# Optimization experiments

Hardware: AMD Instinct MI355X
Metric: run time of the kernel (lower is better)

## Reference

```python
import jax, jax.numpy as jnp
import numpy as np

B, T, D = 4, 2048, 2048
H = 8            # num_heads (= num_kv_heads)
DK = D // H      # head_k_dim = 256
DV = D // H      # head_v_dim = 256
M = 64           # num_slots
GLN = 8.0        # gate_logit_normalizer
EPS = 1e-5
SCALE = 1.0


def swish(x):
    return x * jax.nn.sigmoid(x)


def rms_norm(x, w, eps=EPS):
    var = jnp.mean(jnp.square(x), axis=-1, keepdims=True)
    return x * jax.lax.rsqrt(var + eps) * w


def gsa_scan(q, k, v, s, g, scale):
    # q,k: [B,T,H,DK]; v: [B,T,H,DV]; s,g: [B,T,H,M]
    b, t, h, dk = q.shape
    dv = v.shape[-1]
    m = s.shape[-1]
    xs = tuple(jnp.moveaxis(a, 1, 0) for a in (q, k, v, s, g))  # time-major
    Hk0 = jnp.zeros((b, h, dk, m), q.dtype)
    Hv0 = jnp.zeros((b, h, m, dv), q.dtype)

    def step(carry, inp):
        Hk, Hv = carry
        qt, kt, vt, st, gt = inp
        dec = jnp.exp(gt)                                   # [B,H,M]
        # pass 1: K -> slot state, gate on slot (value) dim
        Hk = Hk * dec[:, :, None, :] + kt[..., :, None] * st[..., None, :]
        o1 = scale * jnp.einsum('bhd,bhdm->bhm', qt, Hk)
        qv = jax.nn.softmax(o1, axis=-1)                    # slot attention
        # pass 2: slot -> V state, gate on slot (key) dim
        Hv = Hv * dec[..., :, None] + st[..., :, None] * vt[..., None, :]
        ot = jnp.einsum('bhm,bhmv->bhv', qv, Hv)
        return (Hk, Hv), ot

    _, oT = jax.lax.scan(step, (Hk0, Hv0), xs)
    return jnp.moveaxis(oT, 0, 1)                           # [B,T,H,DV]


def setup_inputs() -> dict:
    key = jax.random.key(0)
    ks = jax.random.split(key, 8)
    gain = 2.0 ** (-2.5)

    def xavier(k, out_dim, in_dim):
        lim = gain * np.sqrt(6.0 / (in_dim + out_dim))
        return jax.random.uniform(k, (out_dim, in_dim), jnp.float32, -lim, lim)

    return {
        'hidden_states': jax.random.normal(ks[0], (B, T, D), jnp.float32),
        'norm_w': jnp.ones((D,), jnp.float32),
        'q_w': xavier(ks[1], D, D),
        'k_w': xavier(ks[2], D, D),
        'v_w': xavier(ks[3], D, D),
        'f_w': xavier(ks[4], H * M, D),
        'g_norm_w': jnp.ones((D,), jnp.float32),
        'o_w': xavier(ks[5], D, D),
    }


def reference(hidden_states, norm_w, q_w, k_w, v_w, f_w, g_norm_w, o_w):
    x = rms_norm(hidden_states, norm_w)
    q = jnp.einsum('btd,kd->btk', x, q_w).reshape(B, T, H, DK)
    k = jnp.einsum('btd,kd->btk', x, k_w).reshape(B, T, H, DK)
    v = jnp.einsum('btd,kd->btk', x, v_w).reshape(B, T, H, DV)
    f = jnp.einsum('btd,kd->btk', x, f_w).reshape(B, T, H, M)
    q, k = swish(q), swish(k)                 # swish feature map
    v = swish(v)
    f = jax.nn.log_sigmoid(f) / GLN           # log forget gates
    s = 1.0 - jnp.exp(f)                      # slot write strengths
    o = gsa_scan(q, k, v, s, f, SCALE)        # [B,T,H,DV]
    o = o.reshape(B, T, H * DV)
    o = rms_norm(swish(o), g_norm_w)
    return jnp.einsum('btd,kd->btk', o, o_w)
```

## Files before the change

kernel.cpp:

```cpp
#include <hip/hip_runtime.h>
#include <hip/hip_bf16.h>
#include <math.h>


typedef __bf16 bf16x8 __attribute__((ext_vector_type(8)));
typedef float f32x4 __attribute__((ext_vector_type(4)));

#define ROWS 8192
#define DM 2048

#define MODE_F32 0
#define MODE_SWISH 1
#define MODE_GATE 2

#define XS(r, c) ((c) ^ ((r) & 56))

__device__ __forceinline__ float u2f(unsigned short u) {
  union { unsigned int i; float f; } cv; cv.i = ((unsigned int)u) << 16; return cv.f;
}
__device__ __forceinline__ unsigned short f2us(float f) {
  return __builtin_bit_cast(unsigned short, __float2bfloat16(f));
}
__device__ __forceinline__ float swishf(float v) { return v / (1.f + expf(-v)); }

__device__ __forceinline__ void gload16(const void* g, void* l) {
  __builtin_amdgcn_global_load_lds(
      (const __attribute__((address_space(1))) void*)g,
      (__attribute__((address_space(3))) void*)l, 16, 0, 0);
}

__global__ __launch_bounds__(256) void xnorm_kernel(
    const float* __restrict__ in, const float* __restrict__ w,
    unsigned short* __restrict__ out)
{
  const int row = blockIdx.x, tid = threadIdx.x;
  const size_t base = (size_t)row * DM + tid * 8;
  float a[8];
#pragma unroll
  for (int i = 0; i < 8; ++i) a[i] = in[base + i];
  float ss = 0.f;
#pragma unroll
  for (int i = 0; i < 8; ++i) ss += a[i] * a[i];
#pragma unroll
  for (int off = 32; off; off >>= 1) ss += __shfl_xor(ss, off, 64);
  __shared__ float wsum[4];
  if ((tid & 63) == 0) wsum[tid >> 6] = ss;
  __syncthreads();
  float tot = wsum[0] + wsum[1] + wsum[2] + wsum[3];
  float rstd = rsqrtf(tot * (1.f / (float)DM) + 1e-5f);
#pragma unroll
  for (int i = 0; i < 8; ++i)
    out[base + i] = f2us(a[i] * rstd * w[tid * 8 + i]);
}

__global__ __launch_bounds__(256) void oact_norm_kernel(
    const float* __restrict__ o, const float* __restrict__ w,
    unsigned short* __restrict__ out)
{
  const int row = blockIdx.x, tid = threadIdx.x;
  const size_t base = (size_t)row * DM + tid * 8;
  float a[8];
#pragma unroll
  for (int i = 0; i < 8; ++i) a[i] = swishf(o[base + i]);
  float ss = 0.f;
#pragma unroll
  for (int i = 0; i < 8; ++i) ss += a[i] * a[i];
#pragma unroll
  for (int off = 32; off; off >>= 1) ss += __shfl_xor(ss, off, 64);
  __shared__ float wsum[4];
  if ((tid & 63) == 0) wsum[tid >> 6] = ss;
  __syncthreads();
  float tot = wsum[0] + wsum[1] + wsum[2] + wsum[3];
  float rstd = rsqrtf(tot * (1.f / (float)DM) + 1e-5f);
#pragma unroll
  for (int i = 0; i < 8; ++i)
    out[base + i] = f2us(a[i] * rstd * w[tid * 8 + i]);
}

__global__ __launch_bounds__(256) void wconv_kernel(
    const float* __restrict__ in, unsigned short* __restrict__ out)
{
  size_t i = ((size_t)blockIdx.x * 256 + threadIdx.x) * 8;
  float4 a = *(const float4*)(in + i);
  float4 b = *(const float4*)(in + i + 4);
  unsigned short u[8] = {f2us(a.x), f2us(a.y), f2us(a.z), f2us(a.w),
                         f2us(b.x), f2us(b.y), f2us(b.z), f2us(b.w)};
  *(uint4*)(out + i) = *(const uint4*)u;
}

__global__ __launch_bounds__(256) void mgemm2_kernel(
    const unsigned short* __restrict__ A, const unsigned short* __restrict__ WB,
    unsigned short* __restrict__ outB, float* __restrict__ outF,
    int N, int mode)
{
  __shared__ __align__(16) unsigned short As[128 * 32];
  __shared__ __align__(16) unsigned short Bs[128 * 32];
  const int bn = blockIdx.x, bm = blockIdx.y, tid = threadIdx.x;
  const int w = tid >> 6, l = tid & 63;
  const int wm = w & 1, wn = w >> 1;
  const int fr = l & 15, fq = l >> 4;

  f32x4 acc[4][4];
#pragma unroll
  for (int i = 0; i < 4; ++i)
#pragma unroll
    for (int j = 0; j < 4; ++j) acc[i][j] = (f32x4){0.f, 0.f, 0.f, 0.f};

  int prow[2], pcol[2];
#pragma unroll
  for (int j = 0; j < 2; ++j) {
    int p = w * 128 + j * 64 + l;
    prow[j] = p >> 2;
    pcol[j] = ((p & 3) ^ ((prow[j] >> 1) & 3)) * 8;
  }
  const size_t abase = (size_t)(bm * 128) * DM;
  const size_t bbase = (size_t)(bn * 128) * DM;

  for (int k0 = 0; k0 < DM; k0 += 32) {
#pragma unroll
    for (int j = 0; j < 2; ++j) {
      gload16(A + abase + (size_t)prow[j] * DM + k0 + pcol[j],
              &As[(w * 128 + j * 64) * 8]);
      gload16(WB + bbase + (size_t)prow[j] * DM + k0 + pcol[j],
              &Bs[(w * 128 + j * 64) * 8]);
    }
    __syncthreads();
    bf16x8 af[4], bfr[4];
#pragma unroll
    for (int i = 0; i < 4; ++i) {
      int row = wm * 64 + i * 16 + fr;
      af[i] = *(const bf16x8*)&As[row * 32 + ((fq ^ ((row >> 1) & 3)) * 8)];
    }
#pragma unroll
    for (int j = 0; j < 4; ++j) {
      int row = wn * 64 + j * 16 + fr;
      bfr[j] = *(const bf16x8*)&Bs[row * 32 + ((fq ^ ((row >> 1) & 3)) * 8)];
    }
#pragma unroll
    for (int i = 0; i < 4; ++i)
#pragma unroll
      for (int j = 0; j < 4; ++j)
        acc[i][j] = __builtin_amdgcn_mfma_f32_16x16x32_bf16(af[i], bfr[j], acc[i][j], 0, 0, 0);
    __syncthreads();
  }

#pragma unroll
  for (int i = 0; i < 4; ++i) {
#pragma unroll
    for (int rr = 0; rr < 4; ++rr) {
      int row = bm * 128 + wm * 64 + i * 16 + fq * 4 + rr;
#pragma unroll
      for (int j = 0; j < 4; ++j) {
        int col = bn * 128 + wn * 64 + j * 16 + fr;
        float val = acc[i][j][rr];
        size_t idx = (size_t)row * N + col;
        if (mode == MODE_SWISH)      outB[idx] = f2us(swishf(val));
        else if (mode == MODE_F32)   outF[idx] = val;
        else {
          float ls = fminf(val, 0.f) - log1pf(expf(-fabsf(val)));
          outF[idx] = ls * 0.125f;
        }
      }
    }
  }
}

#define BM 128
#define BN 128
#define BK 32
#define LDSP 40

__global__ __launch_bounds__(256) void mgemm_kernel(
    const unsigned short* __restrict__ A, const float* __restrict__ W,
    unsigned short* __restrict__ outB, float* __restrict__ outF,
    int N, int mode)
{
  __shared__ __align__(16) unsigned short As[BM][LDSP];
  __shared__ __align__(16) unsigned short Bs[BN][LDSP];
  const int bn = blockIdx.x, bm = blockIdx.y, tid = threadIdx.x;
  const int w = tid >> 6, l = tid & 63;
  const int wm = w & 1, wn = w >> 1;
  const int fr = l & 15, fq = l >> 4;

  f32x4 acc[4][4];
#pragma unroll
  for (int i = 0; i < 4; ++i)
#pragma unroll
    for (int j = 0; j < 4; ++j) acc[i][j] = (f32x4){0.f, 0.f, 0.f, 0.f};

  for (int k0 = 0; k0 < DM; k0 += BK) {
#pragma unroll
    for (int s = 0; s < 2; ++s) {
      int chunk = tid + s * 256;
      int row = chunk >> 2;
      int cc = (chunk & 3) * 8;
      *(uint4*)&As[row][cc] =
          *(const uint4*)(A + (size_t)(bm * BM + row) * DM + k0 + cc);
    }
#pragma unroll
    for (int s = 0; s < 4; ++s) {
      int chunk = tid + s * 256;
      int row = chunk >> 3;
      int cc = (chunk & 7) * 4;
      float4 wv = *(const float4*)(W + (size_t)(bn * BN + row) * DM + k0 + cc);
      ushort4 w4;
      w4.x = f2us(wv.x); w4.y = f2us(wv.y); w4.z = f2us(wv.z); w4.w = f2us(wv.w);
      *(ushort4*)&Bs[row][cc] = w4;
    }
    __syncthreads();
    bf16x8 af[4], bfr[4];
#pragma unroll
    for (int i = 0; i < 4; ++i) af[i] = *(const bf16x8*)&As[wm * 64 + i * 16 + fr][fq * 8];
#pragma unroll
    for (int j = 0; j < 4; ++j) bfr[j] = *(const bf16x8*)&Bs[wn * 64 + j * 16 + fr][fq * 8];
#pragma unroll
    for (int i = 0; i < 4; ++i)
#pragma unroll
      for (int j = 0; j < 4; ++j)
        acc[i][j] = __builtin_amdgcn_mfma_f32_16x16x32_bf16(af[i], bfr[j], acc[i][j], 0, 0, 0);
    __syncthreads();
  }

#pragma unroll
  for (int i = 0; i < 4; ++i) {
#pragma unroll
    for (int rr = 0; rr < 4; ++rr) {
      int row = bm * BM + wm * 64 + i * 16 + fq * 4 + rr;
#pragma unroll
      for (int j = 0; j < 4; ++j) {
        int col = bn * BN + wn * 64 + j * 16 + fr;
        float val = acc[i][j][rr];
        size_t idx = (size_t)row * N + col;
        if (mode == MODE_SWISH)      outB[idx] = f2us(swishf(val));
        else if (mode == MODE_F32)   outF[idx] = val;
        else {
          float ls = fminf(val, 0.f) - log1pf(expf(-fabsf(val)));
          outF[idx] = ls * 0.125f;
        }
      }
    }
  }
}

template<int NCH, bool INIT>
__global__ __launch_bounds__(512) void gsa_chunk_t(
    const unsigned short* __restrict__ Q, const unsigned short* __restrict__ K,
    const unsigned short* __restrict__ V, const float* __restrict__ G,
    float* __restrict__ O, const float* __restrict__ DK,
    const float* __restrict__ DV)
{
  __shared__ __align__(16) char pool[158848];
  auto EB   = (unsigned short(*)[72])(pool + 0);
  auto O1B  = (unsigned short(*)[72])(pool + 9216);
  auto RB   = (unsigned short(*)[72])(pool + 18432);
  auto RT   = (unsigned short(*)[72])(pool + 27648);
  auto SB   = (unsigned short(*)[72])(pool + 36864);
  auto UB   = (unsigned short(*)[72])(pool + 46080);
  float (*GS)[64] = (float(*)[64])(pool + 55296);
  auto QT   = (unsigned short(*)[264])(pool + 55296);
  auto KTt2 = (unsigned short(*)[72])(pool + 55296);
  auto VTt2 = (unsigned short(*)[72])(pool + 55296);
  auto KT   = (unsigned short(*)[264])(pool + 89088);
  auto VTt1 = (unsigned short(*)[72])(pool + 89088);
  auto GkB  = (unsigned short(*)[264])(pool + 122880);
  auto KTt1 = (unsigned short(*)[72])(pool + 122880);
  auto GvB1 = (unsigned short(*)[72])(pool + 122880);
  auto GvB2 = (unsigned short(*)[72])(pool + 9216);
  float (*red)[68] = (float(*)[68])(pool + 156672);

  int bh, seg;
  if constexpr (INIT) { bh = (int)blockIdx.x >> 3; seg = (int)blockIdx.x & 7; }
  else                { bh = (int)blockIdx.x; seg = 0; }
  const int b = bh >> 3, h = bh & 7;
  const int tid = threadIdx.x;
  const int w = tid >> 6, l = tid & 63, fr = l & 15, fq = l >> 4;
  const int wlo = w & 3, whi = w >> 2;

  f32x4 gk[8], gv[8];
  if constexpr (INIT) {
    const float* dk = DK + ((size_t)bh * 8 + seg) * 16384;
    const float* dv = DV + ((size_t)bh * 8 + seg) * 16384;
#pragma unroll
    for (int jj = 0; jj < 8; ++jj) {
      int ut = (w >= 4 ? 8 : 0) + wlo * 2 + (jj >> 2);
#pragma unroll
      for (int rr = 0; rr < 4; ++rr) {
        gk[jj][rr] = dk[(wlo * 16 + fq * 4 + rr) * 256 + (whi * 8 + jj) * 16 + fr];
        gv[jj][rr] = dv[(ut * 16 + fq * 4 + rr) * 64 + (jj & 3) * 16 + fr];
      }
    }
  } else {
#pragma unroll
    for (int jj = 0; jj < 8; ++jj) {
      gk[jj] = (f32x4){0.f, 0.f, 0.f, 0.f};
      gv[jj] = (f32x4){0.f, 0.f, 0.f, 0.f};
    }
  }

  for (int cl = 0; cl < NCH; ++cl) {
    const int c = seg * NCH + cl;
    const int rowbase = b * 2048 + c * 64;
    const bool upd = (cl != NCH - 1);

#pragma unroll
    for (int s = 0; s < 2; ++s) {
      int id = s * 512 + tid, row = id >> 4, mq = id & 15;
      *(float4*)&GS[row][mq * 4] =
          *(const float4*)&G[(size_t)(rowbase + row) * 512 + h * 64 + mq * 4];
    }
#pragma unroll
    for (int jj = 0; jj < 8; ++jj) {
      int dcol = (whi * 8 + jj) * 16 + fr;
#pragma unroll
      for (int rr = 0; rr < 4; ++rr) {
        int grow = wlo * 16 + fq * 4 + rr;
        GkB[grow][XS(grow, dcol)] = f2us(gk[jj][rr]);
      }
    }
    __syncthreads();

    {
      float ps = 0.f;
#pragma unroll
      for (int j = 0; j < 8; ++j) ps += GS[w * 8 + j][l];
      red[w][l] = ps;
    }
    __syncthreads();

    {
      float cum = 0.f;
      for (int g2 = 0; g2 < w; ++g2) cum += red[g2][l];
#pragma unroll
      for (int j = 0; j < 8; ++j) {
        int i = w * 8 + j;
        float gval = GS[i][l];
        cum += gval;
        float e = expf(cum);
        float s_ = 1.f - expf(gval);
        float r_ = s_ / e;
        EB[i][l] = f2us(e);
        RB[i][XS(i, l)] = f2us(r_);
        RT[l][XS(l, i)] = f2us(r_);
      }
    }
    __syncthreads();

#pragma unroll
    for (int s = 0; s < 4; ++s) {
      int id = s * 512 + tid, row = id >> 5, cc = (id & 31) * 8;
      int sc = XS(row, cc);
      size_t gb = (size_t)(rowbase + row) * 2048 + h * 256 + cc;
      *(uint4*)&QT[row][sc] = *(const uint4*)(Q + gb);
      *(uint4*)&KT[row][sc] = *(const uint4*)(K + gb);
    }
    __syncthreads();

    f32x4 o1acc[2];
    o1acc[0] = (f32x4){0.f, 0.f, 0.f, 0.f};
    o1acc[1] = (f32x4){0.f, 0.f, 0.f, 0.f};
    {
      f32x4 sacc[2];
      sacc[0] = (f32x4){0.f, 0.f, 0.f, 0.f};
      sacc[1] = (f32x4){0.f, 0.f, 0.f, 0.f};
      int ar_ = wlo * 16 + fr;
#pragma unroll
      for (int kk = 0; kk < 8; ++kk) {
        bf16x8 aq = *(const bf16x8*)&QT[ar_][XS(ar_, kk * 32 + fq * 8)];
#pragma unroll
        for (int t2 = 0; t2 < 2; ++t2) {
          int tj = (whi + 2 * t2) * 16 + fr;
          int bc = XS(tj, kk * 32 + fq * 8);
          bf16x8 bk = *(const bf16x8*)&KT[tj][bc];
          sacc[t2] = __builtin_amdgcn_mfma_f32_16x16x32_bf16(aq, bk, sacc[t2], 0, 0, 0);
          bf16x8 bg = *(const bf16x8*)&GkB[tj][bc];
          o1acc[t2] = __builtin_amdgcn_mfma_f32_16x16x32_bf16(aq, bg, o1acc[t2], 0, 0, 0);
        }
      }
#pragma unroll
      for (int t2 = 0; t2 < 2; ++t2)
#pragma unroll
        for (int rr = 0; rr < 4; ++rr) {
          int i = wlo * 16 + fq * 4 + rr;
          int tau = (whi + 2 * t2) * 16 + fr;
          SB[i][XS(i, tau)] = f2us(tau <= i ? sacc[t2][rr] : 0.f);
        }
    }
    __syncthreads();

    {
      int ar_ = wlo * 16 + fr;
#pragma unroll
      for (int kk = 0; kk < 2; ++kk) {
        bf16x8 as = *(const bf16x8*)&SB[ar_][XS(ar_, kk * 32 + fq * 8)];
#pragma unroll
        for (int t2 = 0; t2 < 2; ++t2) {
          int tj = (whi + 2 * t2) * 16 + fr;
          bf16x8 br = *(const bf16x8*)&RT[tj][XS(tj, kk * 32 + fq * 8)];
          o1acc[t2] = __builtin_amdgcn_mfma_f32_16x16x32_bf16(as, br, o1acc[t2], 0, 0, 0);
        }
      }
#pragma unroll
      for (int t2 = 0; t2 < 2; ++t2)
#pragma unroll
        for (int rr = 0; rr < 4; ++rr) {
          int i = wlo * 16 + fq * 4 + rr;
          int m = (whi + 2 * t2) * 16 + fr;
          O1B[i][XS(i, m)] = f2us(u2f(EB[i][m]) * o1acc[t2][rr]);
        }
    }
    __syncthreads();

    {
      int i = tid >> 3, mq = tid & 7;
      int sc = XS(i, mq * 8);
      uint4 raw = *(const uint4*)&O1B[i][sc];
      const unsigned short* rp = (const unsigned short*)&raw;
      float x[8];
#pragma unroll
      for (int j = 0; j < 8; ++j) x[j] = u2f(rp[j]);
      float mx = x[0];
#pragma unroll
      for (int j = 1; j < 8; ++j) mx = fmaxf(mx, x[j]);
      mx = fmaxf(mx, __shfl_xor(mx, 1, 64));
      mx = fmaxf(mx, __shfl_xor(mx, 2, 64));
      mx = fmaxf(mx, __shfl_xor(mx, 4, 64));
      float ex[8], sum = 0.f;
#pragma unroll
      for (int j = 0; j < 8; ++j) { ex[j] = expf(x[j] - mx); sum += ex[j]; }
      sum += __shfl_xor(sum, 1, 64);
      sum += __shfl_xor(sum, 2, 64);
      sum += __shfl_xor(sum, 4, 64);
      float inv = 1.f / sum;
      unsigned short up[8];
#pragma unroll
      for (int j = 0; j < 8; ++j)
        up[j] = f2us(ex[j] * inv * u2f(EB[i][mq * 8 + j]));
      *(uint4*)&UB[i][sc] = *(uint4*)up;
    }
    {
      int m2 = tid >> 3, tq = tid & 7;
      int sc = XS(m2, tq * 8);
      float e63 = u2f(EB[63][m2]);
      uint4 raw = *(const uint4*)&RT[m2][sc];
      const unsigned short* rp = (const unsigned short*)&raw;
      unsigned short ow[8];
#pragma unroll
      for (int j = 0; j < 8; ++j) ow[j] = f2us(u2f(rp[j]) * e63);
      *(uint4*)&RT[m2][sc] = *(uint4*)ow;
    }
    __syncthreads();

    {
      f32x4 pacc[2];
      pacc[0] = (f32x4){0.f, 0.f, 0.f, 0.f};
      pacc[1] = (f32x4){0.f, 0.f, 0.f, 0.f};
      int ar_ = wlo * 16 + fr;
#pragma unroll
      for (int kk = 0; kk < 2; ++kk) {
        bf16x8 ar = *(const bf16x8*)&RB[ar_][XS(ar_, kk * 32 + fq * 8)];
#pragma unroll
        for (int t2 = 0; t2 < 2; ++t2) {
          int tj = (whi + 2 * t2) * 16 + fr;
          bf16x8 bu = *(const bf16x8*)&UB[tj][XS(tj, kk * 32 + fq * 8)];
          pacc[t2] = __builtin_amdgcn_mfma_f32_16x16x32_bf16(ar, bu, pacc[t2], 0, 0, 0);
        }
      }
#pragma unroll
      for (int t2 = 0; t2 < 2; ++t2)
#pragma unroll
        for (int rr = 0; rr < 4; ++rr) {
          int tau = wlo * 16 + fq * 4 + rr;
          int i = (whi + 2 * t2) * 16 + fr;
          SB[i][XS(i, tau)] = f2us(tau <= i ? pacc[t2][rr] : 0.f);
        }
    }
    if (upd) {
#pragma unroll
      for (int s = 0; s < 2; ++s) {
        int id = s * 512 + tid, d8 = id & 15, tau = id >> 4;
        uint4 raw = *(const uint4*)&KT[tau][XS(tau, d8 * 8)];
        const unsigned short* rp = (const unsigned short*)&raw;
#pragma unroll
        for (int j = 0; j < 8; ++j) {
          int trow = d8 * 8 + j;
          KTt1[trow][XS(trow, tau)] = rp[j];
        }
      }
    }
    __syncthreads();

    if (upd) {
      if (w < 4) {
        float e63r[4];
#pragma unroll
        for (int rr = 0; rr < 4; ++rr) e63r[rr] = u2f(EB[63][wlo * 16 + fq * 4 + rr]);
        int wr = wlo * 16 + fr;
        bf16x8 aw0 = *(const bf16x8*)&RT[wr][XS(wr, fq * 8)];
        bf16x8 aw1 = *(const bf16x8*)&RT[wr][XS(wr, 32 + fq * 8)];
#pragma unroll
        for (int jj = 0; jj < 8; ++jj) {
#pragma unroll
          for (int rr = 0; rr < 4; ++rr) gk[jj][rr] *= e63r[rr];
          int kr = jj * 16 + fr;
          bf16x8 bk0 = *(const bf16x8*)&KTt1[kr][XS(kr, fq * 8)];
          bf16x8 bk1 = *(const bf16x8*)&KTt1[kr][XS(kr, 32 + fq * 8)];
          gk[jj] = __builtin_amdgcn_mfma_f32_16x16x32_bf16(aw0, bk0, gk[jj], 0, 0, 0);
          gk[jj] = __builtin_amdgcn_mfma_f32_16x16x32_bf16(aw1, bk1, gk[jj], 0, 0, 0);
        }
      } else {
#pragma unroll
        for (int s = 0; s < 4; ++s) {
          int id = s * 256 + (tid - 256), d8 = id & 15, tau = id >> 4;
          uint4 raw = *(const uint4*)&KT[tau][XS(tau, 128 + d8 * 8)];
          const unsigned short* rp = (const unsigned short*)&raw;
#pragma unroll
          for (int j = 0; j < 8; ++j) {
            int trow = d8 * 8 + j;
            KTt2[trow][XS(trow, tau)] = rp[j];
          }
        }
      }
    }
    __syncthreads();

    if (upd && w >= 4) {
      float e63r[4];
#pragma unroll
      for (int rr = 0; rr < 4; ++rr) e63r[rr] = u2f(EB[63][wlo * 16 + fq * 4 + rr]);
      int wr = wlo * 16 + fr;
      bf16x8 aw0 = *(const bf16x8*)&RT[wr][XS(wr, fq * 8)];
      bf16x8 aw1 = *(const bf16x8*)&RT[wr][XS(wr, 32 + fq * 8)];
#pragma unroll
      for (int jj = 0; jj < 8; ++jj) {
#pragma unroll
        for (int rr = 0; rr < 4; ++rr) gk[jj][rr] *= e63r[rr];
        int kr = jj * 16 + fr;
        bf16x8 bk0 = *(const bf16x8*)&KTt2[kr][XS(kr, fq * 8)];
        bf16x8 bk1 = *(const bf16x8*)&KTt2[kr][XS(kr, 32 + fq * 8)];
        gk[jj] = __builtin_amdgcn_mfma_f32_16x16x32_bf16(aw0, bk0, gk[jj], 0, 0, 0);
        gk[jj] = __builtin_amdgcn_mfma_f32_16x16x32_bf16(aw1, bk1, gk[jj], 0, 0, 0);
      }
    }
    if (w < 4) {
#pragma unroll
      for (int s = 0; s < 4; ++s) {
        int id = s * 256 + tid, u8 = id & 15, tau = id >> 4;
        uint4 raw = *(const uint4*)(V + (size_t)(rowbase + tau) * 2048 + h * 256 + u8 * 8);
        const unsigned short* rp = (const unsigned short*)&raw;
#pragma unroll
        for (int j = 0; j < 8; ++j) {
          int trow = u8 * 8 + j;
          VTt1[trow][XS(trow, tau)] = rp[j];
        }
      }
#pragma unroll
      for (int jj = 0; jj < 8; ++jj) {
        int u0 = (wlo * 2 + (jj >> 2)) * 16 + fq * 4;
        int m = (jj & 3) * 16 + fr;
#pragma unroll
        for (int rr = 0; rr < 4; ++rr) {
          int grow = u0 + rr;
          GvB1[grow][XS(grow, m)] = f2us(gv[jj][rr]);
        }
      }
    }
    __syncthreads();

    {
      int pr = wlo * 16 + fr;
      bf16x8 ap0 = *(const bf16x8*)&SB[pr][XS(pr, fq * 8)];
      bf16x8 ap1 = *(const bf16x8*)&SB[pr][XS(pr, 32 + fq * 8)];
      bf16x8 au0 = *(const bf16x8*)&UB[pr][XS(pr, fq * 8)];
      bf16x8 au1 = *(const bf16x8*)&UB[pr][XS(pr, 32 + fq * 8)];
#pragma unroll
      for (int oo = 0; oo < 4; ++oo) {
        int ut = whi * 4 + oo;
        int vr = ut * 16 + fr;
        f32x4 oa = (f32x4){0.f, 0.f, 0.f, 0.f};
        bf16x8 bv0 = *(const bf16x8*)&VTt1[vr][XS(vr, fq * 8)];
        bf16x8 bv1 = *(const bf16x8*)&VTt1[vr][XS(vr, 32 + fq * 8)];
        bf16x8 bg0 = *(const bf16x8*)&GvB1[vr][XS(vr, fq * 8)];
        bf16x8 bg1 = *(const bf16x8*)&GvB1[vr][XS(vr, 32 + fq * 8)];
        oa = __builtin_amdgcn_mfma_f32_16x16x32_bf16(ap0, bv0, oa, 0, 0, 0);
        oa = __builtin_amdgcn_mfma_f32_16x16x32_bf16(ap1, bv1, oa, 0, 0, 0);
        oa = __builtin_amdgcn_mfma_f32_16x16x32_bf16(au0, bg0, oa, 0, 0, 0);
        oa = __builtin_amdgcn_mfma_f32_16x16x32_bf16(au1, bg1, oa, 0, 0, 0);
#pragma unroll
        for (int rr = 0; rr < 4; ++rr)
          O[(size_t)(rowbase + wlo * 16 + fq * 4 + rr) * 2048 + h * 256 + ut * 16 + fr] = oa[rr];
      }
    }
#pragma unroll
    for (int s = 0; s < 2; ++s) {
      int id = s * 512 + tid, u8 = id & 15, tau = id >> 4;
      uint4 raw = *(const uint4*)(V + (size_t)(rowbase + tau) * 2048 + h * 256 + 128 + u8 * 8);
      const unsigned short* rp = (const unsigned short*)&raw;
#pragma unroll
      for (int j = 0; j < 8; ++j) {
        int trow = u8 * 8 + j;
        VTt2[trow][XS(trow, tau)] = rp[j];
      }
    }
    if (w < 4) {
      if (upd) {
#pragma unroll
        for (int jj = 0; jj < 8; ++jj) {
          int ut = wlo * 2 + (jj >> 2), mt = jj & 3;
          float e63v = u2f(EB[63][mt * 16 + fr]);
#pragma unroll
          for (int rr = 0; rr < 4; ++rr) gv[jj][rr] *= e63v;
          int vr = ut * 16 + fr, br_ = mt * 16 + fr;
          bf16x8 av0 = *(const bf16x8*)&VTt1[vr][XS(vr, fq * 8)];
          bf16x8 av1 = *(const bf16x8*)&VTt1[vr][XS(vr, 32 + fq * 8)];
          bf16x8 bw0 = *(const bf16x8*)&RT[br_][XS(br_, fq * 8)];
          bf16x8 bw1 = *(const bf16x8*)&RT[br_][XS(br_, 32 + fq * 8)];
          gv[jj] = __builtin_amdgcn_mfma_f32_16x16x32_bf16(av0, bw0, gv[jj], 0, 0, 0);
          gv[jj] = __builtin_amdgcn_mfma_f32_16x16x32_bf16(av1, bw1, gv[jj], 0, 0, 0);
        }
      }
    } else {
#pragma unroll
      for (int jj = 0; jj < 8; ++jj) {
        int u0 = (wlo * 2 + (jj >> 2)) * 16 + fq * 4;
        int m = (jj & 3) * 16 + fr;
#pragma unroll
        for (int rr = 0; rr < 4; ++rr) {
          int grow = u0 + rr;
          GvB2[grow][XS(grow, m)] = f2us(gv[jj][rr]);
        }
      }
    }
    __syncthreads();

    {
      int pr = wlo * 16 + fr;
      bf16x8 ap0 = *(const bf16x8*)&SB[pr][XS(pr, fq * 8)];
      bf16x8 ap1 = *(const bf16x8*)&SB[pr][XS(pr, 32 + fq * 8)];
      bf16x8 au0 = *(const bf16x8*)&UB[pr][XS(pr, fq * 8)];
      bf16x8 au1 = *(const bf16x8*)&UB[pr][XS(pr, 32 + fq * 8)];
#pragma unroll
      for (int oo = 0; oo < 4; ++oo) {
        int utl = whi * 4 + oo;
        int vr = utl * 16 + fr;
        f32x4 oa = (f32x4){0.f, 0.f, 0.f, 0.f};
        bf16x8 bv0 = *(const bf16x8*)&VTt2[vr][XS(vr, fq * 8)];
        bf16x8 bv1 = *(const bf16x8*)&VTt2[vr][XS(vr, 32 + fq * 8)];
        bf16x8 bg0 = *(const bf16x8*)&GvB2[vr][XS(vr, fq * 8)];
        bf16x8 bg1 = *(const bf16x8*)&GvB2[vr][XS(vr, 32 + fq * 8)];
        oa = __builtin_amdgcn_mfma_f32_16x16x32_bf16(ap0, bv0, oa, 0, 0, 0);
        oa = __builtin_amdgcn_mfma_f32_16x16x32_bf16(ap1, bv1, oa, 0, 0, 0);
        oa = __builtin_amdgcn_mfma_f32_16x16x32_bf16(au0, bg0, oa, 0, 0, 0);
        oa = __builtin_amdgcn_mfma_f32_16x16x32_bf16(au1, bg1, oa, 0, 0, 0);
#pragma unroll
        for (int rr = 0; rr < 4; ++rr)
          O[(size_t)(rowbase + wlo * 16 + fq * 4 + rr) * 2048 + h * 256 + 128 + utl * 16 + fr] = oa[rr];
      }
    }
    if (upd && w >= 4) {
#pragma unroll
      for (int jj = 0; jj < 8; ++jj) {
        int utl = wlo * 2 + (jj >> 2), mt = jj & 3;
        float e63v = u2f(EB[63][mt * 16 + fr]);
#pragma unroll
        for (int rr = 0; rr < 4; ++rr) gv[jj][rr] *= e63v;
        int vr = utl * 16 + fr, br_ = mt * 16 + fr;
        bf16x8 av0 = *(const bf16x8*)&VTt2[vr][XS(vr, fq * 8)];
        bf16x8 av1 = *(const bf16x8*)&VTt2[vr][XS(vr, 32 + fq * 8)];
        bf16x8 bw0 = *(const bf16x8*)&RT[br_][XS(br_, fq * 8)];
        bf16x8 bw1 = *(const bf16x8*)&RT[br_][XS(br_, 32 + fq * 8)];
        gv[jj] = __builtin_amdgcn_mfma_f32_16x16x32_bf16(av0, bw0, gv[jj], 0, 0, 0);
        gv[jj] = __builtin_amdgcn_mfma_f32_16x16x32_bf16(av1, bw1, gv[jj], 0, 0, 0);
      }
    }
    __syncthreads();
  }
}

__global__ __launch_bounds__(512) void gsa_segA_kernel(
    const unsigned short* __restrict__ K, const unsigned short* __restrict__ V,
    const float* __restrict__ G, float* __restrict__ DK, float* __restrict__ DV,
    float* __restrict__ ES)
{
  __shared__ __align__(16) char pool[135552];
  float (*GS)[64] = (float(*)[64])(pool);
  float (*red)[68] = (float(*)[68])(pool + 16384);
  auto RT   = (unsigned short(*)[72])(pool + 18560);
  float* e63f = (float*)(pool + 27776);
  auto KT   = (unsigned short(*)[264])(pool + 28032);
  auto KTt1 = (unsigned short(*)[72])(pool + 61824);
  auto KTt2 = (unsigned short(*)[72])(pool + 80256);
  auto VTt1 = (unsigned short(*)[72])(pool + 98688);
  auto VTt2 = (unsigned short(*)[72])(pool + 117120);

  const int bh = (int)blockIdx.x >> 3, seg = (int)blockIdx.x & 7;
  const int b = bh >> 3, h = bh & 7;
  const int tid = threadIdx.x;
  const int w = tid >> 6, l = tid & 63, fr = l & 15, fq = l >> 4;
  const int wlo = w & 3, whi = w >> 2;

  f32x4 gk[8], gv[8];
#pragma unroll
  for (int jj = 0; jj < 8; ++jj) {
    gk[jj] = (f32x4){0.f, 0.f, 0.f, 0.f};
    gv[jj] = (f32x4){0.f, 0.f, 0.f, 0.f};
  }
  float gsum = 0.f;

  for (int cl = 0; cl < 4; ++cl) {
    const int rowbase = b * 2048 + (seg * 4 + cl) * 64;

#pragma unroll
    for (int s = 0; s < 2; ++s) {
      int id = s * 512 + tid, row = id >> 4, mq = id & 15;
      *(float4*)&GS[row][mq * 4] =
          *(const float4*)&G[(size_t)(rowbase + row) * 512 + h * 64 + mq * 4];
    }
#pragma unroll
    for (int s = 0; s < 4; ++s) {
      int id = s * 512 + tid, row = id >> 5, cc = (id & 31) * 8;
      *(uint4*)&KT[row][XS(row, cc)] =
          *(const uint4*)(K + (size_t)(rowbase + row) * 2048 + h * 256 + cc);
    }
    __syncthreads();

    {
      float ps = 0.f;
#pragma unroll
      for (int j = 0; j < 8; ++j) ps += GS[w * 8 + j][l];
      red[w][l] = ps;
    }
    __syncthreads();

    {
      float cum = 0.f;
      for (int g2 = 0; g2 < w; ++g2) cum += red[g2][l];
#pragma unroll
      for (int j = 0; j < 8; ++j) {
        int i = w * 8 + j;
        float gval = GS[i][l];
        cum += gval;
        float e = expf(cum);
        float r_ = (1.f - expf(gval)) / e;
        RT[l][XS(l, i)] = f2us(r_);
      }
      if (w == 7) { gsum += cum; e63f[l] = expf(cum); }
    }
    __syncthreads();

    {
      int m2 = tid >> 3, tq = tid & 7;
      int sc = XS(m2, tq * 8);
      float e63 = e63f[m2];
      uint4 raw = *(const uint4*)&RT[m2][sc];
      const unsigned short* rp = (const unsigned short*)&raw;
      unsigned short ow[8];
#pragma unroll
      for (int j = 0; j < 8; ++j) ow[j] = f2us(u2f(rp[j]) * e63);
      *(uint4*)&RT[m2][sc] = *(uint4*)ow;
    }
#pragma unroll
    for (int s = 0; s < 2; ++s) {
      int id = s * 512 + tid, d8 = id & 15, tau = id >> 4;
      uint4 raw1 = *(const uint4*)&KT[tau][XS(tau, d8 * 8)];
      uint4 raw2 = *(const uint4*)&KT[tau][XS(tau, 128 + d8 * 8)];
      const unsigned short* rp1 = (const unsigned short*)&raw1;
      const unsigned short* rp2 = (const unsigned short*)&raw2;
#pragma unroll
      for (int j = 0; j < 8; ++j) {
        int trow = d8 * 8 + j;
        KTt1[trow][XS(trow, tau)] = rp1[j];
        KTt2[trow][XS(trow, tau)] = rp2[j];
      }
    }
#pragma unroll
    for (int s = 0; s < 2; ++s) {
      int id = s * 512 + tid, u8 = id & 15, tau = id >> 4;
      size_t gb = (size_t)(rowbase + tau) * 2048 + h * 256 + u8 * 8;
      uint4 raw1 = *(const uint4*)(V + gb);
      uint4 raw2 = *(const uint4*)(V + gb + 128);
      const unsigned short* rp1 = (const unsigned short*)&raw1;
      const unsigned short* rp2 = (const unsigned short*)&raw2;
#pragma unroll
      for (int j = 0; j < 8; ++j) {
        int trow = u8 * 8 + j;
        VTt1[trow][XS(trow, tau)] = rp1[j];
        VTt2[trow][XS(trow, tau)] = rp2[j];
      }
    }
    __syncthreads();

    {
      float e63r[4];
#pragma unroll
      for (int rr = 0; rr < 4; ++rr) e63r[rr] = e63f[wlo * 16 + fq * 4 + rr];
      int wr = wlo * 16 + fr;
      bf16x8 aw0 = *(const bf16x8*)&RT[wr][XS(wr, fq * 8)];
      bf16x8 aw1 = *(const bf16x8*)&RT[wr][XS(wr, 32 + fq * 8)];
      auto KTx = (w < 4) ? KTt1 : KTt2;
#pragma unroll
      for (int jj = 0; jj < 8; ++jj) {
#pragma unroll
        for (int rr = 0; rr < 4; ++rr) gk[jj][rr] *= e63r[rr];
        int kr = jj * 16 + fr;
        bf16x8 bk0 = *(const bf16x8*)&KTx[kr][XS(kr, fq * 8)];
        bf16x8 bk1 = *(const bf16x8*)&KTx[kr][XS(kr, 32 + fq * 8)];
        gk[jj] = __builtin_amdgcn_mfma_f32_16x16x32_bf16(aw0, bk0, gk[jj], 0, 0, 0);
        gk[jj] = __builtin_amdgcn_mfma_f32_16x16x32_bf16(aw1, bk1, gk[jj], 0, 0, 0);
      }
      auto VTx = (w < 4) ? VTt1 : VTt2;
#pragma unroll
      for (int jj = 0; jj < 8; ++jj) {
        int utl = wlo * 2 + (jj >> 2), mt = jj & 3;
        float e63v = e63f[mt * 16 + fr];
#pragma unroll
        for (int rr = 0; rr < 4; ++rr) gv[jj][rr] *= e63v;
        int vr = utl * 16 + fr, br_ = mt * 16 + fr;
        bf16x8 av0 = *(const bf16x8*)&VTx[vr][XS(vr, fq * 8)];
        bf16x8 av1 = *(const bf16x8*)&VTx[vr][XS(vr, 32 + fq * 8)];
        bf16x8 bw0 = *(const bf16x8*)&RT[br_][XS(br_, fq * 8)];
        bf16x8 bw1 = *(const bf16x8*)&RT[br_][XS(br_, 32 + fq * 8)];
        gv[jj] = __builtin_amdgcn_mfma_f32_16x16x32_bf16(av0, bw0, gv[jj], 0, 0, 0);
        gv[jj] = __builtin_amdgcn_mfma_f32_16x16x32_bf16(av1, bw1, gv[jj], 0, 0, 0);
      }
    }
    __syncthreads();
  }

  float* dk = DK + ((size_t)bh * 8 + seg) * 16384;
  float* dv = DV + ((size_t)bh * 8 + seg) * 16384;
#pragma unroll
  for (int jj = 0; jj < 8; ++jj) {
    int ut = (w >= 4 ? 8 : 0) + wlo * 2 + (jj >> 2);
#pragma unroll
    for (int rr = 0; rr < 4; ++rr) {
      dk[(wlo * 16 + fq * 4 + rr) * 256 + (whi * 8 + jj) * 16 + fr] = gk[jj][rr];
      dv[(ut * 16 + fq * 4 + rr) * 64 + (jj & 3) * 16 + fr] = gv[jj][rr];
    }
  }
  if (w == 7) ES[((size_t)bh * 8 + seg) * 64 + l] = expf(gsum);
}

__global__ __launch_bounds__(1024) void gsa_segB_kernel(
    float* __restrict__ DK, float* __restrict__ DV, const float* __restrict__ ES)
{
  const int bh = blockIdx.x, tid = threadIdx.x;
  __shared__ float es[8][64];
  if (tid < 512) es[tid >> 6][tid & 63] = ES[(size_t)bh * 512 + tid];
  __syncthreads();
  float* dk = DK + (size_t)bh * 8 * 16384;
  float* dv = DV + (size_t)bh * 8 * 16384;
  for (int k = 0; k < 16; ++k) {
    int e = k * 1024 + tid;
    int m = e >> 8;
    float S = 0.f;
#pragma unroll
    for (int s = 0; s < 8; ++s) {
      float d = dk[s * 16384 + e];
      dk[s * 16384 + e] = S;
      S = fmaf(S, es[s][m], d);
    }
  }
  for (int k = 0; k < 16; ++k) {
    int e = k * 1024 + tid;
    int m = e & 63;
    float S = 0.f;
#pragma unroll
    for (int s = 0; s < 8; ++s) {
      float d = dv[s * 16384 + e];
      dv[s * 16384 + e] = S;
      S = fmaf(S, es[s][m], d);
    }
  }
}

__global__ __launch_bounds__(256) void fillf_kernel(float* o, float v) {
  o[(size_t)blockIdx.x * 256 + threadIdx.x] = v;
}

extern "C" void kernel_launch(void* const* d_in, const int* in_sizes, int n_in,
                              void* d_out, int out_size, void* d_ws, size_t ws_size,
                              hipStream_t stream)
{
  const float* hidden   = (const float*)d_in[0];
  const float* norm_w   = (const float*)d_in[1];
  const float* q_w      = (const float*)d_in[2];
  const float* k_w      = (const float*)d_in[3];
  const float* v_w      = (const float*)d_in[4];
  const float* f_w      = (const float*)d_in[5];
  const float* g_norm_w = (const float*)d_in[6];
  const float* o_w      = (const float*)d_in[7];

  float* dout = (float*)d_out;
  char* ws = (char*)d_ws;
  const size_t SZB = (size_t)ROWS * DM * 2;
  const size_t SZG = (size_t)ROWS * 512 * 4;
  const size_t NEED = 4 * SZB + SZG;
  const size_t SZD = (size_t)32 * 8 * 16384 * 4;
  const size_t NEED_BIG = NEED + 2 * SZD + (size_t)32 * 8 * 64 * 4;
  const size_t SZWB = (size_t)DM * DM * 2;
  const size_t SZWF = (size_t)512 * DM * 2;
  const size_t NEED_W = NEED_BIG + 4 * SZWB + SZWF;

  if (ws_size < NEED) {
    fillf_kernel<<<65536, 256, 0, stream>>>(dout, 123.0f);
    return;
  }

  unsigned short* XN = (unsigned short*)(ws);
  unsigned short* Qb = (unsigned short*)(ws + SZB);
  unsigned short* Kb = (unsigned short*)(ws + 2 * SZB);
  unsigned short* Vb = (unsigned short*)(ws + 3 * SZB);
  float* Gb          = (float*)(ws + 4 * SZB);
  float* DK          = (float*)(ws + NEED);
  float* DV          = DK + (size_t)32 * 8 * 16384;
  float* ES          = DV + (size_t)32 * 8 * 16384;
  unsigned short* WQ = (unsigned short*)(ws + NEED_BIG);
  unsigned short* WK = WQ + SZWB / 2;
  unsigned short* WV = WK + SZWB / 2;
  unsigned short* WO = WV + SZWB / 2;
  unsigned short* WF = WO + SZWB / 2;

  xnorm_kernel<<<ROWS, 256, 0, stream>>>(hidden, norm_w, XN);

  if (ws_size >= NEED_W) {
    wconv_kernel<<<2048, 256, 0, stream>>>(q_w, WQ);
    wconv_kernel<<<2048, 256, 0, stream>>>(k_w, WK);
    wconv_kernel<<<2048, 256, 0, stream>>>(v_w, WV);
    wconv_kernel<<<2048, 256, 0, stream>>>(o_w, WO);
    wconv_kernel<<<512, 256, 0, stream>>>(f_w, WF);

    mgemm2_kernel<<<dim3(16, 64), 256, 0, stream>>>(XN, WQ, Qb, nullptr, 2048, MODE_SWISH);
    mgemm2_kernel<<<dim3(16, 64), 256, 0, stream>>>(XN, WK, Kb, nullptr, 2048, MODE_SWISH);
    mgemm2_kernel<<<dim3(16, 64), 256, 0, stream>>>(XN, WV, Vb, nullptr, 2048, MODE_SWISH);
    mgemm2_kernel<<<dim3(4, 64), 256, 0, stream>>>(XN, WF, nullptr, Gb, 512, MODE_GATE);
  } else {
    mgemm_kernel<<<dim3(16, 64), 256, 0, stream>>>(XN, q_w, Qb, nullptr, 2048, MODE_SWISH);
    mgemm_kernel<<<dim3(16, 64), 256, 0, stream>>>(XN, k_w, Kb, nullptr, 2048, MODE_SWISH);
    mgemm_kernel<<<dim3(16, 64), 256, 0, stream>>>(XN, v_w, Vb, nullptr, 2048, MODE_SWISH);
    mgemm_kernel<<<dim3(4, 64), 256, 0, stream>>>(XN, f_w, nullptr, Gb, 512, MODE_GATE);
  }

  if (ws_size >= NEED_BIG) {
    gsa_segA_kernel<<<256, 512, 0, stream>>>(Kb, Vb, Gb, DK, DV, ES);
    gsa_segB_kernel<<<32, 1024, 0, stream>>>(DK, DV, ES);
    gsa_chunk_t<4, true><<<256, 512, 0, stream>>>(Qb, Kb, Vb, Gb, dout, DK, DV);
  } else {
    gsa_chunk_t<32, false><<<32, 512, 0, stream>>>(Qb, Kb, Vb, Gb, dout, nullptr, nullptr);
  }

  oact_norm_kernel<<<ROWS, 256, 0, stream>>>(dout, g_norm_w, XN);

  if (ws_size >= NEED_W)
    mgemm2_kernel<<<dim3(16, 64), 256, 0, stream>>>(XN, WO, nullptr, dout, 2048, MODE_F32);
  else
    mgemm_kernel<<<dim3(16, 64), 256, 0, stream>>>(XN, o_w, nullptr, dout, 2048, MODE_F32);
}
```

Before: 946.6 us.

## Prefetch next chunk's Q/K/V/G into registers and swizzle GEMM block order

```diff
diff --git a/kernel.cpp b/kernel.cpp
--- a/kernel.cpp
+++ b/kernel.cpp
@@ -95,7 +95,12 @@
 {
   __shared__ __align__(16) unsigned short As[128 * 32];
   __shared__ __align__(16) unsigned short Bs[128 * 32];
-  const int bn = blockIdx.x, bm = blockIdx.y, tid = threadIdx.x;
+  const int tid = threadIdx.x;
+  const int bid = (int)(blockIdx.y * gridDim.x + blockIdx.x);
+  const int nwg = (int)(gridDim.x * gridDim.y);
+  const int cpx = nwg >> 3;
+  const int swz = (bid & 7) * cpx + (bid >> 3);
+  const int bn = swz % (int)gridDim.x, bm = swz / (int)gridDim.x;
   const int w = tid >> 6, l = tid & 63;
   const int wm = w & 1, wn = w >> 1;
   const int fr = l & 15, fq = l >> 4;
@@ -276,6 +281,46 @@
   const int w = tid >> 6, l = tid & 63, fr = l & 15, fq = l >> 4;
   const int wlo = w & 3, whi = w >> 2;
 
+  float4 pg[2];
+  uint4 pq[4], pk[4], pv1[4], pv2[2];
+  auto pref_g = [&](int c) {
+    const int rb = b * 2048 + c * 64;
+#pragma unroll
+    for (int s = 0; s < 2; ++s) {
+      int id = s * 512 + tid, row = id >> 4, mq = id & 15;
+      pg[s] = *(const float4*)&G[(size_t)(rb + row) * 512 + h * 64 + mq * 4];
+    }
+  };
+  auto pref_qk = [&](int c) {
+    const int rb = b * 2048 + c * 64;
+#pragma unroll
+    for (int s = 0; s < 4; ++s) {
+      int id = s * 512 + tid, row = id >> 5, cc = (id & 31) * 8;
+      size_t gb = (size_t)(rb + row) * 2048 + h * 256 + cc;
+      pq[s] = *(const uint4*)(Q + gb);
+      pk[s] = *(const uint4*)(K + gb);
+    }
+  };
+  auto pref_v = [&](int c) {
+    const int rb = b * 2048 + c * 64;
+    if (tid < 256) {
+#pragma unroll
+      for (int s = 0; s < 4; ++s) {
+        int id = s * 256 + tid, u8 = id & 15, tau = id >> 4;
+        pv1[s] = *(const uint4*)(V + (size_t)(rb + tau) * 2048 + h * 256 + u8 * 8);
+      }
+    }
+#pragma unroll
+    for (int s = 0; s < 2; ++s) {
+      int id = s * 512 + tid, u8 = id & 15, tau = id >> 4;
+      pv2[s] = *(const uint4*)(V + (size_t)(rb + tau) * 2048 + h * 256 + 128 + u8 * 8);
+    }
+  };
+
+  pref_g(seg * NCH);
+  pref_qk(seg * NCH);
+  pref_v(seg * NCH);
+
   f32x4 gk[8], gv[8];
   if constexpr (INIT) {
     const float* dk = DK + ((size_t)bh * 8 + seg) * 16384;
@@ -305,8 +350,7 @@
 #pragma unroll
     for (int s = 0; s < 2; ++s) {
       int id = s * 512 + tid, row = id >> 4, mq = id & 15;
-      *(float4*)&GS[row][mq * 4] =
-          *(const float4*)&G[(size_t)(rowbase + row) * 512 + h * 64 + mq * 4];
+      *(float4*)&GS[row][mq * 4] = pg[s];
     }
 #pragma unroll
     for (int jj = 0; jj < 8; ++jj) {
@@ -349,11 +393,12 @@
     for (int s = 0; s < 4; ++s) {
       int id = s * 512 + tid, row = id >> 5, cc = (id & 31) * 8;
       int sc = XS(row, cc);
-      size_t gb = (size_t)(rowbase + row) * 2048 + h * 256 + cc;
-      *(uint4*)&QT[row][sc] = *(const uint4*)(Q + gb);
-      *(uint4*)&KT[row][sc] = *(const uint4*)(K + gb);
-    }
-    __syncthreads();
+      *(uint4*)&QT[row][sc] = pq[s];
+      *(uint4*)&KT[row][sc] = pk[s];
+    }
+    __syncthreads();
+
+    if (cl + 1 < NCH) { pref_g(c + 1); pref_qk(c + 1); }
 
     f32x4 o1acc[2];
     o1acc[0] = (f32x4){0.f, 0.f, 0.f, 0.f};
@@ -545,8 +590,7 @@
 #pragma unroll
       for (int s = 0; s < 4; ++s) {
         int id = s * 256 + tid, u8 = id & 15, tau = id >> 4;
-        uint4 raw = *(const uint4*)(V + (size_t)(rowbase + tau) * 2048 + h * 256 + u8 * 8);
-        const unsigned short* rp = (const unsigned short*)&raw;
+        const unsigned short* rp = (const unsigned short*)&pv1[s];
 #pragma unroll
         for (int j = 0; j < 8; ++j) {
           int trow = u8 * 8 + j;
@@ -593,14 +637,14 @@
 #pragma unroll
     for (int s = 0; s < 2; ++s) {
       int id = s * 512 + tid, u8 = id & 15, tau = id >> 4;
-      uint4 raw = *(const uint4*)(V + (size_t)(rowbase + tau) * 2048 + h * 256 + 128 + u8 * 8);
-      const unsigned short* rp = (const unsigned short*)&raw;
+      const unsigned short* rp = (const unsigned short*)&pv2[s];
 #pragma unroll
       for (int j = 0; j < 8; ++j) {
         int trow = u8 * 8 + j;
         VTt2[trow][XS(trow, tau)] = rp[j];
       }
     }
+    if (cl + 1 < NCH) pref_v(c + 1);
     if (w < 4) {
       if (upd) {
 #pragma unroll
@@ -698,6 +742,34 @@
   const int w = tid >> 6, l = tid & 63, fr = l & 15, fq = l >> 4;
   const int wlo = w & 3, whi = w >> 2;
 
+  float4 pg[2];
+  uint4 pk[4], pv[4];
+  auto pref_gk = [&](int cl) {
+    const int rb = b * 2048 + (seg * 4 + cl) * 64;
+#pragma unroll
+    for (int s = 0; s < 2; ++s) {
+      int id = s * 512 + tid, row = id >> 4, mq = id & 15;
+      pg[s] = *(const float4*)&G[(size_t)(rb + row) * 512 + h * 64 + mq * 4];
+    }
+#pragma unroll
+    for (int s = 0; s < 4; ++s) {
+      int id = s * 512 + tid, row = id >> 5, cc = (id & 31) * 8;
+      pk[s] = *(const uint4*)(K + (size_t)(rb + row) * 2048 + h * 256 + cc);
+    }
+  };
+  auto pref_v = [&](int cl) {
+    const int rb = b * 2048 + (seg * 4 + cl) * 64;
+#pragma unroll
+    for (int s = 0; s < 2; ++s) {
+      int id = s * 512 + tid, u8 = id & 15, tau = id >> 4;
+      size_t gb = (size_t)(rb + tau) * 2048 + h * 256 + u8 * 8;
+      pv[s * 2]     = *(const uint4*)(V + gb);
+      pv[s * 2 + 1] = *(const uint4*)(V + gb + 128);
+    }
+  };
+  pref_gk(0);
+  pref_v(0);
+
   f32x4 gk[8], gv[8];
 #pragma unroll
   for (int jj = 0; jj < 8; ++jj) {
@@ -707,21 +779,19 @@
   float gsum = 0.f;
 
   for (int cl = 0; cl < 4; ++cl) {
-    const int rowbase = b * 2048 + (seg * 4 + cl) * 64;
-
 #pragma unroll
     for (int s = 0; s < 2; ++s) {
       int id = s * 512 + tid, row = id >> 4, mq = id & 15;
-      *(float4*)&GS[row][mq * 4] =
-          *(const float4*)&G[(size_t)(rowbase + row) * 512 + h * 64 + mq * 4];
+      *(float4*)&GS[row][mq * 4] = pg[s];
     }
 #pragma unroll
     for (int s = 0; s < 4; ++s) {
       int id = s * 512 + tid, row = id >> 5, cc = (id & 31) * 8;
-      *(uint4*)&KT[row][XS(row, cc)] =
-          *(const uint4*)(K + (size_t)(rowbase + row) * 2048 + h * 256 + cc);
-    }
-    __syncthreads();
+      *(uint4*)&KT[row][XS(row, cc)] = pk[s];
+    }
+    __syncthreads();
+
+    if (cl + 1 < 4) pref_gk(cl + 1);
 
     {
       float ps = 0.f;
@@ -775,11 +845,8 @@
 #pragma unroll
     for (int s = 0; s < 2; ++s) {
       int id = s * 512 + tid, u8 = id & 15, tau = id >> 4;
-      size_t gb = (size_t)(rowbase + tau) * 2048 + h * 256 + u8 * 8;
-      uint4 raw1 = *(const uint4*)(V + gb);
-      uint4 raw2 = *(const uint4*)(V + gb + 128);
-      const unsigned short* rp1 = (const unsigned short*)&raw1;
-      const unsigned short* rp2 = (const unsigned short*)&raw2;
+      const unsigned short* rp1 = (const unsigned short*)&pv[s * 2];
+      const unsigned short* rp2 = (const unsigned short*)&pv[s * 2 + 1];
 #pragma unroll
       for (int j = 0; j < 8; ++j) {
         int trow = u8 * 8 + j;
@@ -787,6 +854,7 @@
         VTt2[trow][XS(trow, tau)] = rp2[j];
       }
     }
+    if (cl + 1 < 4) pref_v(cl + 1);
     __syncthreads();
 
     {
```

Result: slower. 1.024 ms (+8.2%).

## Fuse Q/K/V/gate projection GEMMs into one launch with XCD-aware block swizzle

Applied to the files above, without the earlier changes.

```diff
diff --git a/kernel.cpp b/kernel.cpp
--- a/kernel.cpp
+++ b/kernel.cpp
@@ -95,7 +95,12 @@
 {
   __shared__ __align__(16) unsigned short As[128 * 32];
   __shared__ __align__(16) unsigned short Bs[128 * 32];
-  const int bn = blockIdx.x, bm = blockIdx.y, tid = threadIdx.x;
+  const int tid = threadIdx.x;
+  const int bid = (int)(blockIdx.y * gridDim.x + blockIdx.x);
+  const int nwg = (int)(gridDim.x * gridDim.y);
+  const int cpx = nwg >> 3;
+  const int swz = (bid & 7) * cpx + (bid >> 3);
+  const int bn = swz % (int)gridDim.x, bm = swz / (int)gridDim.x;
   const int w = tid >> 6, l = tid & 63;
   const int wm = w & 1, wn = w >> 1;
   const int fr = l & 15, fq = l >> 4;
@@ -159,6 +164,91 @@
         else {
           float ls = fminf(val, 0.f) - log1pf(expf(-fabsf(val)));
           outF[idx] = ls * 0.125f;
+        }
+      }
+    }
+  }
+}
+
+__global__ __launch_bounds__(256) void mgemm2_fused_kernel(
+    const unsigned short* __restrict__ A, const unsigned short* __restrict__ WALL,
+    unsigned short* __restrict__ Qb, unsigned short* __restrict__ Kb,
+    unsigned short* __restrict__ Vb, float* __restrict__ Gb)
+{
+  __shared__ __align__(16) unsigned short As[128 * 32];
+  __shared__ __align__(16) unsigned short Bs[128 * 32];
+  const int tid = threadIdx.x;
+  const int bid = (int)(blockIdx.y * gridDim.x + blockIdx.x);
+  const int nwg = (int)(gridDim.x * gridDim.y);
+  const int cpx = nwg >> 3;
+  const int swz = (bid & 7) * cpx + (bid >> 3);
+  const int bn = swz % (int)gridDim.x, bm = swz / (int)gridDim.x;
+  const int w = tid >> 6, l = tid & 63;
+  const int wm = w & 1, wn = w >> 1;
+  const int fr = l & 15, fq = l >> 4;
+
+  f32x4 acc[4][4];
+#pragma unroll
+  for (int i = 0; i < 4; ++i)
+#pragma unroll
+    for (int j = 0; j < 4; ++j) acc[i][j] = (f32x4){0.f, 0.f, 0.f, 0.f};
+
+  int prow[2], pcol[2];
+#pragma unroll
+  for (int j = 0; j < 2; ++j) {
+    int p = w * 128 + j * 64 + l;
+    prow[j] = p >> 2;
+    pcol[j] = ((p & 3) ^ ((prow[j] >> 1) & 3)) * 8;
+  }
+  const size_t abase = (size_t)(bm * 128) * DM;
+  const size_t bbase = (size_t)(bn * 128) * DM;
+
+  for (int k0 = 0; k0 < DM; k0 += 32) {
+#pragma unroll
+    for (int j = 0; j < 2; ++j) {
+      gload16(A + abase + (size_t)prow[j] * DM + k0 + pcol[j],
+              &As[(w * 128 + j * 64) * 8]);
+      gload16(WALL + bbase + (size_t)prow[j] * DM + k0 + pcol[j],
+              &Bs[(w * 128 + j * 64) * 8]);
+    }
+    __syncthreads();
+    bf16x8 af[4], bfr[4];
+#pragma unroll
+    for (int i = 0; i < 4; ++i) {
+      int row = wm * 64 + i * 16 + fr;
+      af[i] = *(const bf16x8*)&As[row * 32 + ((fq ^ ((row >> 1) & 3)) * 8)];
+    }
+#pragma unroll
+    for (int j = 0; j < 4; ++j) {
+      int row = wn * 64 + j * 16 + fr;
+      bfr[j] = *(const bf16x8*)&Bs[row * 32 + ((fq ^ ((row >> 1) & 3)) * 8)];
+    }
+#pragma unroll
+    for (int i = 0; i < 4; ++i)
+#pragma unroll
+      for (int j = 0; j < 4; ++j)
+        acc[i][j] = __builtin_amdgcn_mfma_f32_16x16x32_bf16(af[i], bfr[j], acc[i][j], 0, 0, 0);
+    __syncthreads();
+  }
+
+  const int tgt = bn >> 4;
+  unsigned short* oB = (tgt == 0) ? Qb : (tgt == 1) ? Kb : Vb;
+  const int coff = tgt * 2048;
+
+#pragma unroll
+  for (int i = 0; i < 4; ++i) {
+#pragma unroll
+    for (int rr = 0; rr < 4; ++rr) {
+      int row = bm * 128 + wm * 64 + i * 16 + fq * 4 + rr;
+#pragma unroll
+      for (int j = 0; j < 4; ++j) {
+        int colg = bn * 128 + wn * 64 + j * 16 + fr;
+        float val = acc[i][j][rr];
+        if (tgt < 3) {
+          oB[(size_t)row * 2048 + (colg - coff)] = f2us(swishf(val));
+        } else {
+          float ls = fminf(val, 0.f) - log1pf(expf(-fabsf(val)));
+          Gb[(size_t)row * 512 + (colg - 6144)] = ls * 0.125f;
         }
       }
     }
@@ -915,10 +1005,10 @@
   float* DV          = DK + (size_t)32 * 8 * 16384;
   float* ES          = DV + (size_t)32 * 8 * 16384;
   unsigned short* WQ = (unsigned short*)(ws + NEED_BIG);
-  unsigned short* WK = WQ + SZWB / 2;
-  unsigned short* WV = WK + SZWB / 2;
-  unsigned short* WO = WV + SZWB / 2;
-  unsigned short* WF = WO + SZWB / 2;
+  unsigned short* WK = WQ + (size_t)2048 * 2048;
+  unsigned short* WV = WK + (size_t)2048 * 2048;
+  unsigned short* WF = WV + (size_t)2048 * 2048;
+  unsigned short* WO = WF + (size_t)512 * 2048;
 
   xnorm_kernel<<<ROWS, 256, 0, stream>>>(hidden, norm_w, XN);
 
@@ -926,13 +1016,10 @@
     wconv_kernel<<<2048, 256, 0, stream>>>(q_w, WQ);
     wconv_kernel<<<2048, 256, 0, stream>>>(k_w, WK);
     wconv_kernel<<<2048, 256, 0, stream>>>(v_w, WV);
+    wconv_kernel<<<512, 256, 0, stream>>>(f_w, WF);
     wconv_kernel<<<2048, 256, 0, stream>>>(o_w, WO);
-    wconv_kernel<<<512, 256, 0, stream>>>(f_w, WF);
-
-    mgemm2_kernel<<<dim3(16, 64), 256, 0, stream>>>(XN, WQ, Qb, nullptr, 2048, MODE_SWISH);
-    mgemm2_kernel<<<dim3(16, 64), 256, 0, stream>>>(XN, WK, Kb, nullptr, 2048, MODE_SWISH);
-    mgemm2_kernel<<<dim3(16, 64), 256, 0, stream>>>(XN, WV, Vb, nullptr, 2048, MODE_SWISH);
-    mgemm2_kernel<<<dim3(4, 64), 256, 0, stream>>>(XN, WF, nullptr, Gb, 512, MODE_GATE);
+
+    mgemm2_fused_kernel<<<dim3(52, 64), 256, 0, stream>>>(XN, WQ, Qb, Kb, Vb, Gb);
   } else {
     mgemm_kernel<<<dim3(16, 64), 256, 0, stream>>>(XN, q_w, Qb, nullptr, 2048, MODE_SWISH);
     mgemm_kernel<<<dim3(16, 64), 256, 0, stream>>>(XN, k_w, Kb, nullptr, 2048, MODE_SWISH);
```

New measurement: 851.6 us. 10.0% less time.
